# Kernel optimization log

Hardware: AMD Instinct MI355X
Metric: run time of the kernel (lower is better)

## Reference

```python
import jax, jax.numpy as jnp
import numpy as np

N_TYPES = 4
N_REL = 8
N_HEADS = 8
IN_DIM = 256
N_HID = 128
D_K = N_HID // N_HEADS
N_LAYERS = 2
N_NODES = 100000
N_EDGES = 400000


def setup_inputs() -> dict:
    key = jax.random.key(0)
    ks = jax.random.split(key, 24)
    s = 0.05
    inp = {
        'node_feature': jax.random.normal(ks[0], (N_NODES, IN_DIM), jnp.float32),
        'node_type': jax.random.randint(ks[1], (N_NODES,), 0, N_TYPES),
        'edge_index': jax.random.randint(ks[2], (2, N_EDGES), 0, N_NODES),
        'edge_type': jax.random.randint(ks[3], (N_EDGES,), 0, N_REL),
        # per-type input adapters
        'adapt_w': jax.random.normal(ks[4], (N_TYPES, IN_DIM, N_HID), jnp.float32) * s,
        'adapt_b': jnp.zeros((N_TYPES, N_HID), jnp.float32),
        # HGT conv params, stacked over layers
        'k_w': jax.random.normal(ks[5], (N_LAYERS, N_TYPES, N_HID, N_HID), jnp.float32) * s,
        'k_b': jnp.zeros((N_LAYERS, N_TYPES, N_HID), jnp.float32),
        'q_w': jax.random.normal(ks[6], (N_LAYERS, N_TYPES, N_HID, N_HID), jnp.float32) * s,
        'q_b': jnp.zeros((N_LAYERS, N_TYPES, N_HID), jnp.float32),
        'v_w': jax.random.normal(ks[7], (N_LAYERS, N_TYPES, N_HID, N_HID), jnp.float32) * s,
        'v_b': jnp.zeros((N_LAYERS, N_TYPES, N_HID), jnp.float32),
        'a_w': jax.random.normal(ks[8], (N_LAYERS, N_TYPES, N_HID, N_HID), jnp.float32) * s,
        'a_b': jnp.zeros((N_LAYERS, N_TYPES, N_HID), jnp.float32),
        'rel_pri': jnp.ones((N_LAYERS, N_REL, N_HEADS), jnp.float32),
        'rel_att': jnp.tile(jnp.eye(D_K, dtype=jnp.float32), (N_LAYERS, N_REL, N_HEADS, 1, 1))
                   + jax.random.normal(ks[9], (N_LAYERS, N_REL, N_HEADS, D_K, D_K), jnp.float32) * s,
        'rel_msg': jnp.tile(jnp.eye(D_K, dtype=jnp.float32), (N_LAYERS, N_REL, N_HEADS, 1, 1))
                   + jax.random.normal(ks[10], (N_LAYERS, N_REL, N_HEADS, D_K, D_K), jnp.float32) * s,
        'skip': jnp.ones((N_LAYERS, N_TYPES), jnp.float32),
    }
    return inp


def _per_type_linear(x, w, b, node_type, n_idx):
    # x: [N, din], w: [T, din, dout], b: [T, dout] -> gather row for each node's type
    h_all = jnp.einsum('ni,tio->tno', x, w) + b[:, None, :]  # [T, N, dout]
    return h_all[node_type, n_idx]  # [N, dout]


def _edge_softmax(score, tgt, n):
    # score: [E, H]; softmax over incoming edges of each target node
    m = jax.ops.segment_max(score, tgt, num_segments=n)  # [N, H]
    e = jnp.exp(score - m[tgt])
    z = jax.ops.segment_sum(e, tgt, num_segments=n)
    return e / (z[tgt] + 1e-9)


def _hgt_layer(x, node_type, src, tgt, edge_type,
               kw, kb, qw, qb, vw, vb, aw, ab, pri, att_m, msg_m, skip):
    n = x.shape[0]
    n_idx = jnp.arange(n)
    k = _per_type_linear(x, kw, kb, node_type, n_idx).reshape(n, N_HEADS, D_K)
    q = _per_type_linear(x, qw, qb, node_type, n_idx).reshape(n, N_HEADS, D_K)
    v = _per_type_linear(x, vw, vb, node_type, n_idx).reshape(n, N_HEADS, D_K)
    k_src, v_src, q_tgt = k[src], v[src], q[tgt]  # [E, H, dk]
    # per-relation attention/message transforms, accumulated over small fixed R
    k_rel = jnp.zeros_like(k_src)
    v_rel = jnp.zeros_like(v_src)
    for r in range(N_REL):
        msk = (edge_type == r)[:, None, None]
        k_rel = k_rel + jnp.einsum('ehd,hdf->ehf', jnp.where(msk, k_src, 0.0), att_m[r])
        v_rel = v_rel + jnp.einsum('ehd,hdf->ehf', jnp.where(msk, v_src, 0.0), msg_m[r])
    score = (q_tgt * k_rel).sum(-1) * pri[edge_type] * (1.0 / (D_K ** 0.5))  # [E, H]
    att = _edge_softmax(score, tgt, n)
    agg = jax.ops.segment_sum(att[..., None] * v_rel, tgt, num_segments=n)  # [N, H, dk]
    agg = agg.reshape(n, N_HID)
    trans = _per_type_linear(jax.nn.gelu(agg), aw, ab, node_type, n_idx)
    alpha = jax.nn.sigmoid(skip)[node_type][:, None]
    return trans * alpha + x * (1.0 - alpha)


def reference(node_feature, node_type, edge_index, edge_type,
              adapt_w, adapt_b, k_w, k_b, q_w, q_b, v_w, v_b,
              a_w, a_b, rel_pri, rel_att, rel_msg, skip):
    n = node_feature.shape[0]
    n_idx = jnp.arange(n)
    # per-node-type adapter + tanh (gather-linear-scatter, fully vectorized)
    h = jnp.tanh(_per_type_linear(node_feature, adapt_w, adapt_b, node_type, n_idx))
    src, tgt = edge_index[0], edge_index[1]
    for l in range(N_LAYERS):
        h = _hgt_layer(h, node_type, src, tgt, edge_type,
                       k_w[l], k_b[l], q_w[l], q_b[l], v_w[l], v_b[l],
                       a_w[l], a_b[l], rel_pri[l], rel_att[l], rel_msg[l], skip[l])
    return h
```

## Files before the change

### kernel.cpp

```cpp
#include <hip/hip_runtime.h>
#include <math.h>

constexpr int N_TYPES = 4;
constexpr int N_REL   = 8;
constexpr int N_HEADS = 8;
constexpr int IN_DIM  = 256;
constexpr int N_HID   = 128;
constexpr int D_K     = 16;
constexpr int N_LAYERS= 2;
constexpr int NN      = 100000;
constexpr int NE      = 400000;
constexpr int NBLK    = (NN + 255) / 256;

__device__ __forceinline__ float gelu_f(float x) {
    const float c = 0.7978845608028654f;
    float x3 = x * x * x;
    return 0.5f * x * (1.0f + tanhf(c * (x + 0.044715f * x3)));
}
__device__ __forceinline__ float sigmoid_f(float x) {
    return 1.0f / (1.0f + expf(-x));
}

__global__ __launch_bounds__(256) void count2_kernel(
    const int* __restrict__ ntype, const int* __restrict__ tgt,
    unsigned* ncnt, unsigned* tcnt)
{
    int i = blockIdx.x * 256 + threadIdx.x;
    int lane = threadIdx.x & 63;
    int t = (i < NN) ? ntype[i] : -1;
    #pragma unroll
    for (int tt = 0; tt < N_TYPES; tt++) {
        unsigned long long m = __ballot(t == tt);
        if (m != 0ull && lane == __ffsll((unsigned long long)m) - 1)
            atomicAdd(&ncnt[tt], (unsigned)__popcll(m));
    }
    if (i < NE) atomicAdd(&tcnt[tgt[i]], 1u);
}

__global__ void node_offsets_kernel(unsigned* c)
{
    unsigned a = 0;
    for (int t = 0; t < N_TYPES; t++) { c[8 + t] = a; c[4 + t] = a; a += c[t]; }
    c[8 + N_TYPES] = a;
}

__global__ __launch_bounds__(256) void scan1_kernel(
    const unsigned* __restrict__ cnt, unsigned* __restrict__ eoff,
    unsigned* __restrict__ bsum)
{
    __shared__ unsigned sh[256];
    int i = blockIdx.x * 256 + threadIdx.x;
    unsigned v = (i < NN) ? cnt[i] : 0u;
    sh[threadIdx.x] = v;
    __syncthreads();
    for (int off = 1; off < 256; off <<= 1) {
        unsigned add = (threadIdx.x >= off) ? sh[threadIdx.x - off] : 0u;
        __syncthreads();
        sh[threadIdx.x] += add;
        __syncthreads();
    }
    if (i < NN) eoff[i] = sh[threadIdx.x] - v;
    if (threadIdx.x == 255) bsum[blockIdx.x] = sh[255];
}

__global__ __launch_bounds__(512) void scan2_kernel(unsigned* __restrict__ bsum)
{
    __shared__ unsigned sh[512];
    int i = threadIdx.x;
    unsigned v = (i < NBLK) ? bsum[i] : 0u;
    sh[i] = v;
    __syncthreads();
    for (int off = 1; off < 512; off <<= 1) {
        unsigned add = (i >= off) ? sh[i - off] : 0u;
        __syncthreads();
        sh[i] += add;
        __syncthreads();
    }
    if (i < NBLK) bsum[i] = sh[i] - v;
}

__global__ __launch_bounds__(256) void scan3_kernel(
    unsigned* __restrict__ eoff, const unsigned* __restrict__ bsum,
    unsigned* __restrict__ ecur)
{
    int i = blockIdx.x * 256 + threadIdx.x;
    if (i < NN) {
        unsigned v = eoff[i] + bsum[blockIdx.x];
        eoff[i] = v;
        ecur[i] = v;
    }
    if (i == 0) eoff[NN] = (unsigned)NE;
}

__global__ __launch_bounds__(256) void scatter2_kernel(
    const int* __restrict__ ntype,
    const int* __restrict__ src, const int* __restrict__ tgt,
    const int* __restrict__ etype,
    unsigned* ncur, unsigned* ecur,
    int* __restrict__ nidx,
    int* __restrict__ er_t)
{
    int i = blockIdx.x * 256 + threadIdx.x;
    int lane = threadIdx.x & 63;
    int t = (i < NN) ? ntype[i] : -1;
    #pragma unroll
    for (int tt = 0; tt < N_TYPES; tt++) {
        unsigned long long m = __ballot(t == tt);
        if (m == 0ull) continue;
        int leader = __ffsll((unsigned long long)m) - 1;
        unsigned base = 0;
        if (lane == leader) base = atomicAdd(&ncur[tt], (unsigned)__popcll(m));
        base = __shfl(base, leader, 64);
        if (t == tt) {
            unsigned rank = (unsigned)__popcll(m & ((1ull << lane) - 1ull));
            nidx[base + rank] = i;
        }
    }
    if (i < NE) {
        int tg = tgt[i];
        unsigned p = atomicAdd(&ecur[tg], 1u);
        er_t[p] = (src[i] << 3) | etype[i];
    }
}

template<int DIN, int MIN, int MOUT>
__global__ __launch_bounds__(256) void ptl128_kernel(
    const float* __restrict__ x,
    const int* __restrict__ nidx,
    const unsigned* __restrict__ noff,
    const float* __restrict__ W,
    const float* __restrict__ Bb,
    const float* __restrict__ skipv,
    const float* __restrict__ hprev,
    float* __restrict__ out)
{
    constexpr int BK = 32;
    const int t = blockIdx.y;
    const unsigned s0 = noff[t], s1 = noff[t + 1];
    const unsigned base = s0 + blockIdx.x * 128u;
    if (base >= s1) return;
    const int nrows = (int)min(128u, s1 - base);

    __shared__ __align__(16) float xs[BK][128];
    __shared__ __align__(16) float wsl[BK][128];
    __shared__ int nid[128];

    const int tid = threadIdx.x;
    if (tid < 128) nid[tid] = nidx[base + (unsigned)min(tid, nrows - 1)];
    __syncthreads();

    const int tx = tid & 15;
    const int ty = tid >> 4;
    const int row = tid & 127, kg = tid >> 7;

    float acc[8][8];
    #pragma unroll
    for (int m = 0; m < 8; m++)
        #pragma unroll
        for (int j = 0; j < 8; j++) acc[m][j] = 0.0f;

    const float* Wt = W + (size_t)t * DIN * 128;

    for (int k0 = 0; k0 < DIN; k0 += BK) {
        {
            const float* xp = x + (size_t)nid[row] * DIN + k0 + kg * 16;
            float4 a0 = ((const float4*)xp)[0];
            float4 a1 = ((const float4*)xp)[1];
            float4 a2 = ((const float4*)xp)[2];
            float4 a3 = ((const float4*)xp)[3];
            float v[16] = {a0.x, a0.y, a0.z, a0.w, a1.x, a1.y, a1.z, a1.w,
                           a2.x, a2.y, a2.z, a2.w, a3.x, a3.y, a3.z, a3.w};
            #pragma unroll
            for (int i = 0; i < 16; i++) {
                float q = v[i];
                if (MIN == 1) q = gelu_f(q);
                xs[kg * 16 + i][row] = q;
            }
        }
        {
            const float* wp = Wt + (size_t)k0 * 128 + tid * 16;
            #pragma unroll
            for (int i = 0; i < 4; i++)
                *(float4*)&wsl[0][tid * 16 + 4 * i] = ((const float4*)wp)[i];
        }
        __syncthreads();
        #pragma unroll 8
        for (int kk = 0; kk < BK; kk++) {
            float4 xa = *(float4*)&xs[kk][ty * 8];
            float4 xb = *(float4*)&xs[kk][ty * 8 + 4];
            float4 wa = *(float4*)&wsl[kk][tx * 8];
            float4 wb = *(float4*)&wsl[kk][tx * 8 + 4];
            float xv[8] = {xa.x, xa.y, xa.z, xa.w, xb.x, xb.y, xb.z, xb.w};
            float wv[8] = {wa.x, wa.y, wa.z, wa.w, wb.x, wb.y, wb.z, wb.w};
            #pragma unroll
            for (int m = 0; m < 8; m++)
                #pragma unroll
                for (int j = 0; j < 8; j++)
                    acc[m][j] += xv[m] * wv[j];
        }
        __syncthreads();
    }

    float alpha = 0.0f;
    if (MOUT == 2) alpha = sigmoid_f(skipv[t]);
    float bb[8];
    #pragma unroll
    for (int j = 0; j < 8; j++) bb[j] = Bb[t * 128 + tx * 8 + j];

    #pragma unroll
    for (int m = 0; m < 8; m++) {
        int rr = ty * 8 + m;
        if (rr < nrows) {
            int n = nid[rr];
            float o[8];
            #pragma unroll
            for (int j = 0; j < 8; j++) o[j] = acc[m][j] + bb[j];
            if (MOUT == 0) {
                #pragma unroll
                for (int j = 0; j < 8; j++) o[j] = tanhf(o[j]);
            } else if (MOUT == 2) {
                const float* hp = hprev + (size_t)n * 128 + tx * 8;
                float4 h0 = *(const float4*)(hp);
                float4 h1 = *(const float4*)(hp + 4);
                float hv[8] = {h0.x, h0.y, h0.z, h0.w, h1.x, h1.y, h1.z, h1.w};
                #pragma unroll
                for (int j = 0; j < 8; j++)
                    o[j] = o[j] * alpha + hv[j] * (1.0f - alpha);
            }
            float* op = out + (size_t)n * 128 + tx * 8;
            *(float4*)(op)     = make_float4(o[0], o[1], o[2], o[3]);
            *(float4*)(op + 4) = make_float4(o[4], o[5], o[6], o[7]);
        }
    }
}

__global__ __launch_bounds__(256) void hgt_edge_fused(
    const int* __restrict__ er_t,
    const unsigned* __restrict__ eoff,
    const float* __restrict__ kbuf,
    const float* __restrict__ vbuf,
    const float* __restrict__ att,
    const float* __restrict__ msg,
    const float* __restrict__ pri,
    float* __restrict__ qagg)
{
    __shared__ float aq_lds[2][1024];
    __shared__ float pv_lds[2][1024];
    const int tid  = threadIdx.x;
    const int tsel = tid >> 7;
    const int li   = tid & 127;
    const int h    = li >> 4;
    const int j    = li & 15;
    const int l    = tid & 63;
    const int hb   = tid & 0x30;
    const int t    = blockIdx.x * 2 + tsel;
    if (t >= NN) return;

    const unsigned e0 = eoff[t];
    const unsigned e1 = eoff[t + 1];
    const int deg = (int)(e1 - e0);

    if (deg == 0) {
        qagg[(size_t)t * 128 + li] = 0.0f;
        return;
    }

    float* al = aq_lds[tsel];
    float* pl = pv_lds[tsel];

    #pragma unroll
    for (int r = 0; r < 8; r++) pl[r * 128 + li] = 0.0f;

    const float qo = qagg[(size_t)t * 128 + li];
    float qh[16];
    #pragma unroll
    for (int f = 0; f < 16; f++) qh[f] = __shfl(qo, hb + f, 64);

    int pkl = 0;
    if (l < 16 && e0 + (unsigned)l < e1) pkl = er_t[e0 + l];

    const int dc = min(deg, 16);
    unsigned mask = 0;
    for (int c = 0; c < dc; ++c) mask |= 1u << (__shfl(pkl, c, 64) & 7);
    for (unsigned e = e0 + 16; e < e1; ++e) mask |= 1u << (er_t[e] & 7);

    unsigned need = mask;
    while (need) {
        const int r = __ffs(need) - 1; need &= need - 1;
        const float* Ar = att + (((r * 8 + h) * 16 + j) * 16);
        float4 A0 = ((const float4*)Ar)[0];
        float4 A1 = ((const float4*)Ar)[1];
        float4 A2 = ((const float4*)Ar)[2];
        float4 A3 = ((const float4*)Ar)[3];
        float acc =
            A0.x*qh[0]  + A0.y*qh[1]  + A0.z*qh[2]  + A0.w*qh[3]  +
            A1.x*qh[4]  + A1.y*qh[5]  + A1.z*qh[6]  + A1.w*qh[7]  +
            A2.x*qh[8]  + A2.y*qh[9]  + A2.z*qh[10] + A2.w*qh[11] +
            A3.x*qh[12] + A3.y*qh[13] + A3.z*qh[14] + A3.w*qh[15];
        al[r * 128 + li] = acc * pri[r * 8 + h] * 0.25f;
    }

    float z = 0.0f;
    float* plp = pl + li;
    const float* alp = al + li;
    const float* kb = kbuf + li;
    const float* vb = vbuf + li;

    unsigned e = e0;
    for (; e + 4 <= e1; e += 4) {
        const int o = (int)(e - e0);
        int p0, p1, p2, p3;
        if (o + 3 < 16) {
            p0 = __shfl(pkl, o + 0, 64);
            p1 = __shfl(pkl, o + 1, 64);
            p2 = __shfl(pkl, o + 2, 64);
            p3 = __shfl(pkl, o + 3, 64);
        } else {
            p0 = er_t[e + 0]; p1 = er_t[e + 1];
            p2 = er_t[e + 2]; p3 = er_t[e + 3];
        }
        const int o0 = (p0 & ~7) << 4;
        const int o1 = (p1 & ~7) << 4;
        const int o2 = (p2 & ~7) << 4;
        const int o3 = (p3 & ~7) << 4;
        const float k0 = kb[o0]; const float v0 = vb[o0];
        const float k1 = kb[o1]; const float v1 = vb[o1];
        const float k2 = kb[o2]; const float v2 = vb[o2];
        const float k3 = kb[o3]; const float v3 = vb[o3];
        float s0 = k0 * alp[(p0 & 7) * 128];
        float s1 = k1 * alp[(p1 & 7) * 128];
        float s2 = k2 * alp[(p2 & 7) * 128];
        float s3 = k3 * alp[(p3 & 7) * 128];
        s0 += __shfl_xor(s0, 1); s1 += __shfl_xor(s1, 1);
        s2 += __shfl_xor(s2, 1); s3 += __shfl_xor(s3, 1);
        s0 += __shfl_xor(s0, 2); s1 += __shfl_xor(s1, 2);
        s2 += __shfl_xor(s2, 2); s3 += __shfl_xor(s3, 2);
        s0 += __shfl_xor(s0, 4); s1 += __shfl_xor(s1, 4);
        s2 += __shfl_xor(s2, 4); s3 += __shfl_xor(s3, 4);
        s0 += __shfl_xor(s0, 8); s1 += __shfl_xor(s1, 8);
        s2 += __shfl_xor(s2, 8); s3 += __shfl_xor(s3, 8);
        const float q0 = __expf(s0 - 8.0f);
        const float q1 = __expf(s1 - 8.0f);
        const float q2 = __expf(s2 - 8.0f);
        const float q3 = __expf(s3 - 8.0f);
        z += q0 + q1 + q2 + q3;
        plp[(p0 & 7) * 128] += q0 * v0;
        plp[(p1 & 7) * 128] += q1 * v1;
        plp[(p2 & 7) * 128] += q2 * v2;
        plp[(p3 & 7) * 128] += q3 * v3;
    }
    if (e + 2 <= e1) {
        const int o = (int)(e - e0);
        int p0, p1;
        if (o + 1 < 16) { p0 = __shfl(pkl, o, 64); p1 = __shfl(pkl, o + 1, 64); }
        else            { p0 = er_t[e]; p1 = er_t[e + 1]; }
        const int o0 = (p0 & ~7) << 4;
        const int o1 = (p1 & ~7) << 4;
        const float k0 = kb[o0]; const float v0 = vb[o0];
        const float k1 = kb[o1]; const float v1 = vb[o1];
        float s0 = k0 * alp[(p0 & 7) * 128];
        float s1 = k1 * alp[(p1 & 7) * 128];
        s0 += __shfl_xor(s0, 1); s1 += __shfl_xor(s1, 1);
        s0 += __shfl_xor(s0, 2); s1 += __shfl_xor(s1, 2);
        s0 += __shfl_xor(s0, 4); s1 += __shfl_xor(s1, 4);
        s0 += __shfl_xor(s0, 8); s1 += __shfl_xor(s1, 8);
        const float q0 = __expf(s0 - 8.0f);
        const float q1 = __expf(s1 - 8.0f);
        z += q0 + q1;
        plp[(p0 & 7) * 128] += q0 * v0;
        plp[(p1 & 7) * 128] += q1 * v1;
        e += 2;
    }
    if (e < e1) {
        const int o = (int)(e - e0);
        const int p0 = (o < 16) ? __shfl(pkl, o, 64) : er_t[e];
        const int o0 = (p0 & ~7) << 4;
        const float k0 = kb[o0]; const float v0 = vb[o0];
        float s0 = k0 * alp[(p0 & 7) * 128];
        s0 += __shfl_xor(s0, 1);
        s0 += __shfl_xor(s0, 2);
        s0 += __shfl_xor(s0, 4);
        s0 += __shfl_xor(s0, 8);
        const float q0 = __expf(s0 - 8.0f);
        z += q0;
        plp[(p0 & 7) * 128] += q0 * v0;
    }

    float acc = 0.0f;
    for (int r = 0; r < 8; r++) {
        if (!((mask >> r) & 1)) continue;
        const float* Mr = msg + ((r * 8 + h) * 256) + j;
        const float* sb = pl + r * 128 + h * 16;
        #pragma unroll
        for (int d = 0; d < 16; d++)
            acc += sb[d] * Mr[d * 16];
    }
    qagg[(size_t)t * 128 + li] = acc * __frcp_rn(z + 1e-9f);
}

extern "C" void kernel_launch(void* const* d_in, const int* in_sizes, int n_in,
                              void* d_out, int out_size, void* d_ws, size_t ws_size,
                              hipStream_t stream)
{
    const float* node_feature = (const float*)d_in[0];
    const int*   node_type    = (const int*)d_in[1];
    const int*   edge_index   = (const int*)d_in[2];
    const int*   edge_type    = (const int*)d_in[3];
    const float* adapt_w      = (const float*)d_in[4];
    const float* adapt_b      = (const float*)d_in[5];
    const float* k_w = (const float*)d_in[6];
    const float* k_b = (const float*)d_in[7];
    const float* q_w = (const float*)d_in[8];
    const float* q_b = (const float*)d_in[9];
    const float* v_w = (const float*)d_in[10];
    const float* v_b = (const float*)d_in[11];
    const float* a_w = (const float*)d_in[12];
    const float* a_b = (const float*)d_in[13];
    const float* rel_pri = (const float*)d_in[14];
    const float* rel_att = (const float*)d_in[15];
    const float* rel_msg = (const float*)d_in[16];
    const float* skip    = (const float*)d_in[17];

    const int* src = edge_index;
    const int* tgt = edge_index + NE;

    float* OUT = (float*)d_out;

    char* w = (char*)d_ws;
    auto alloc = [&](size_t bytes) -> void* {
        void* p = (void*)w;
        w += (bytes + 255) & ~(size_t)255;
        return p;
    };
    float*    B0    = (float*)alloc((size_t)NN * 128 * 4);
    float*    B1    = (float*)alloc((size_t)NN * 128 * 4);
    float*    B2    = (float*)alloc((size_t)NN * 128 * 4);
    int*      nidx  = (int*)alloc((size_t)NN * 4);
    int*      er_t  = (int*)alloc((size_t)NE * 4);
    unsigned* tcnt  = (unsigned*)alloc((size_t)NN * 4);
    unsigned* eoff  = (unsigned*)alloc((size_t)(NN + 1) * 4);
    unsigned* ecur  = (unsigned*)alloc((size_t)NN * 4);
    unsigned* bsum  = (unsigned*)alloc((size_t)NBLK * 4);
    unsigned* cnts  = (unsigned*)alloc(16 * 4);

    unsigned* ncnt = cnts;
    unsigned* ncur = cnts + 4;
    unsigned* noff = cnts + 8;

    hipMemsetAsync(cnts, 0, 16 * 4, stream);
    hipMemsetAsync(tcnt, 0, (size_t)NN * 4, stream);

    const int gblocks = (NE + 255) / 256;
    count2_kernel<<<gblocks, 256, 0, stream>>>(node_type, tgt, ncnt, tcnt);
    node_offsets_kernel<<<1, 1, 0, stream>>>(cnts);
    scan1_kernel<<<NBLK, 256, 0, stream>>>(tcnt, eoff, bsum);
    scan2_kernel<<<1, 512, 0, stream>>>(bsum);
    scan3_kernel<<<NBLK, 256, 0, stream>>>(eoff, bsum, ecur);
    scatter2_kernel<<<gblocks, 256, 0, stream>>>(node_type, src, tgt, edge_type,
                                                 ncur, ecur, nidx, er_t);

    dim3 pgrid((NN + 127) / 128, N_TYPES);
    ptl128_kernel<IN_DIM, 0, 0><<<pgrid, 256, 0, stream>>>(
        node_feature, nidx, noff, adapt_w, adapt_b, nullptr, nullptr, B0);

    const int fblocks = (NN + 1) / 2;

    for (int l = 0; l < N_LAYERS; l++) {
        float* hin  = l ? B1 : B0;
        float* kb_  = l ? B0 : B1;
        float* qb_  = B2;
        float* vb_  = OUT;
        float* hout = l ? OUT : B1;

        const float* kwl = k_w + (size_t)l * N_TYPES * 128 * 128;
        const float* kbl = k_b + (size_t)l * N_TYPES * 128;
        const float* qwl = q_w + (size_t)l * N_TYPES * 128 * 128;
        const float* qbl = q_b + (size_t)l * N_TYPES * 128;
        const float* vwl = v_w + (size_t)l * N_TYPES * 128 * 128;
        const float* vbl = v_b + (size_t)l * N_TYPES * 128;
        const float* awl = a_w + (size_t)l * N_TYPES * 128 * 128;
        const float* abl = a_b + (size_t)l * N_TYPES * 128;
        const float* pril = rel_pri + (size_t)l * N_REL * N_HEADS;
        const float* attl = rel_att + (size_t)l * N_REL * N_HEADS * D_K * D_K;
        const float* msgl = rel_msg + (size_t)l * N_REL * N_HEADS * D_K * D_K;
        const float* skipl = skip + (size_t)l * N_TYPES;

        ptl128_kernel<N_HID, 0, 1><<<pgrid, 256, 0, stream>>>(
            hin, nidx, noff, kwl, kbl, nullptr, nullptr, kb_);
        ptl128_kernel<N_HID, 0, 1><<<pgrid, 256, 0, stream>>>(
            hin, nidx, noff, qwl, qbl, nullptr, nullptr, qb_);
        ptl128_kernel<N_HID, 0, 1><<<pgrid, 256, 0, stream>>>(
            hin, nidx, noff, vwl, vbl, nullptr, nullptr, vb_);

        hgt_edge_fused<<<fblocks, 256, 0, stream>>>(
            er_t, eoff, kb_, vb_, attl, msgl, pril, qb_);

        ptl128_kernel<N_HID, 1, 2><<<pgrid, 256, 0, stream>>>(
            qb_, nidx, noff, awl, abl, skipl, hin, hout);
    }
}
```

Measured before the change: 1.205 ms.

## Run per-type 128-wide linears on bf16x3 MFMA with split hi/lo operands

Replaces the FP32 SIMT per-type linear kernels for K/Q/V and the output projection with an MFMA kernel. It keeps near-FP32 accuracy by splitting each operand into bf16 hi and lo parts and summing three products. Activations are converted (with GELU fused for the output projection) by a separate pass, and the weights are pre-transposed and split once per call. This targets the matrix-core throughput gap, at the cost of extra conversion passes and extra memory traffic for the split copies.

```diff
diff --git a/kernel.cpp b/kernel.cpp
--- a/kernel.cpp
+++ b/kernel.cpp
@@ -12,6 +12,9 @@
 constexpr int NE      = 400000;
 constexpr int NBLK    = (NN + 255) / 256;
 
+typedef __attribute__((ext_vector_type(8))) short bf16x8;
+typedef __attribute__((ext_vector_type(4))) float f32x4;
+
 __device__ __forceinline__ float gelu_f(float x) {
     const float c = 0.7978845608028654f;
     float x3 = x * x * x;
@@ -121,6 +124,54 @@
         unsigned p = atomicAdd(&ecur[tg], 1u);
         er_t[p] = (src[i] << 3) | etype[i];
     }
+}
+
+__device__ __forceinline__ void split_bf16(float q, ushort& hi, ushort& lo) {
+    unsigned u = __float_as_uint(q);
+    hi = (ushort)(u >> 16);
+    float hf = __uint_as_float(u & 0xFFFF0000u);
+    lo = (ushort)(__float_as_uint(q - hf) >> 16);
+}
+
+template<int GELU>
+__global__ __launch_bounds__(256) void cvt_x_kernel(
+    const float* __restrict__ x, ushort* __restrict__ xh,
+    ushort* __restrict__ xl, int total4)
+{
+    int gid = blockIdx.x * 256 + threadIdx.x;
+    if (gid >= total4) return;
+    float4 v = ((const float4*)x)[gid];
+    float a[4] = {v.x, v.y, v.z, v.w};
+    ushort h[4], lo[4];
+    #pragma unroll
+    for (int i = 0; i < 4; i++) {
+        float q = a[i];
+        if (GELU) q = gelu_f(q);
+        split_bf16(q, h[i], lo[i]);
+    }
+    uint2 hp, lp;
+    hp.x = (unsigned)h[0] | ((unsigned)h[1] << 16);
+    hp.y = (unsigned)h[2] | ((unsigned)h[3] << 16);
+    lp.x = (unsigned)lo[0] | ((unsigned)lo[1] << 16);
+    lp.y = (unsigned)lo[2] | ((unsigned)lo[3] << 16);
+    ((uint2*)xh)[gid] = hp;
+    ((uint2*)xl)[gid] = lp;
+}
+
+__global__ __launch_bounds__(256) void cvt_wT_kernel(
+    const float* __restrict__ W, ushort* __restrict__ whT,
+    ushort* __restrict__ wlT, int din)
+{
+    int gid = blockIdx.x * 256 + threadIdx.x;
+    int tot = 4 * din * 128;
+    if (gid >= tot) return;
+    int t = gid / (din * 128);
+    int rem = gid - t * din * 128;
+    int k = rem >> 7, n = rem & 127;
+    ushort hi, lo;
+    split_bf16(W[gid], hi, lo);
+    size_t o = ((size_t)t * 128 + n) * din + k;
+    whT[o] = hi; wlT[o] = lo;
 }
 
 template<int DIN, int MIN, int MOUT>
@@ -230,6 +281,111 @@
             float* op = out + (size_t)n * 128 + tx * 8;
             *(float4*)(op)     = make_float4(o[0], o[1], o[2], o[3]);
             *(float4*)(op + 4) = make_float4(o[4], o[5], o[6], o[7]);
+        }
+    }
+}
+
+template<int DIN, int MOUT>
+__global__ __launch_bounds__(256) void mfma_ptl_kernel(
+    const ushort* __restrict__ xh, const ushort* __restrict__ xl,
+    const int* __restrict__ nidx, const unsigned* __restrict__ noff,
+    const ushort* __restrict__ whT, const ushort* __restrict__ wlT,
+    const float* __restrict__ Bb,
+    const float* __restrict__ skipv, const float* __restrict__ hprev,
+    float* __restrict__ out)
+{
+    const int t = blockIdx.y;
+    const unsigned s0 = noff[t], s1 = noff[t + 1];
+    const unsigned base = s0 + blockIdx.x * 128u;
+    if (base >= s1) return;
+    const int nrows = (int)min(128u, s1 - base);
+
+    __shared__ __align__(16) ushort xsh[128][40];
+    __shared__ __align__(16) ushort xsl2[128][40];
+    __shared__ __align__(16) ushort wsh[128][40];
+    __shared__ __align__(16) ushort wsl2[128][40];
+    __shared__ int nid[128];
+
+    const int tid = threadIdx.x;
+    if (tid < 128) nid[tid] = nidx[base + (unsigned)min(tid, nrows - 1)];
+    __syncthreads();
+
+    const int lane = tid & 63;
+    const int wave = tid >> 6;
+    const int wr = wave >> 1, wc = wave & 1;
+    const int lm = lane & 15, lk = lane >> 4;
+
+    f32x4 acc[4][4];
+    #pragma unroll
+    for (int a = 0; a < 4; a++)
+        #pragma unroll
+        for (int b = 0; b < 4; b++)
+            acc[a][b] = (f32x4){0.0f, 0.0f, 0.0f, 0.0f};
+
+    const ushort* WhT = whT + (size_t)t * 128 * DIN;
+    const ushort* WlT = wlT + (size_t)t * 128 * DIN;
+
+    const int srow = tid & 127, shalf = tid >> 7;
+    const size_t xoff = (size_t)nid[srow] * DIN;
+
+    for (int k0 = 0; k0 < DIN; k0 += 32) {
+        {
+            const ushort* ph  = xh + xoff + k0 + shalf * 16;
+            const ushort* pl2 = xl + xoff + k0 + shalf * 16;
+            *(uint4*)&xsh[srow][shalf * 16]      = *(const uint4*)ph;
+            *(uint4*)&xsh[srow][shalf * 16 + 8]  = *(const uint4*)(ph + 8);
+            *(uint4*)&xsl2[srow][shalf * 16]     = *(const uint4*)pl2;
+            *(uint4*)&xsl2[srow][shalf * 16 + 8] = *(const uint4*)(pl2 + 8);
+            const ushort* qh = WhT + (size_t)srow * DIN + k0 + shalf * 16;
+            const ushort* ql = WlT + (size_t)srow * DIN + k0 + shalf * 16;
+            *(uint4*)&wsh[srow][shalf * 16]      = *(const uint4*)qh;
+            *(uint4*)&wsh[srow][shalf * 16 + 8]  = *(const uint4*)(qh + 8);
+            *(uint4*)&wsl2[srow][shalf * 16]     = *(const uint4*)ql;
+            *(uint4*)&wsl2[srow][shalf * 16 + 8] = *(const uint4*)(ql + 8);
+        }
+        __syncthreads();
+        bf16x8 ah[4], alo[4];
+        #pragma unroll
+        for (int fm = 0; fm < 4; fm++) {
+            int row = wr * 64 + fm * 16 + lm;
+            ah[fm]  = *(const bf16x8*)&xsh[row][lk * 8];
+            alo[fm] = *(const bf16x8*)&xsl2[row][lk * 8];
+        }
+        #pragma unroll
+        for (int fn = 0; fn < 4; fn++) {
+            int col = wc * 64 + fn * 16 + lm;
+            bf16x8 bh = *(const bf16x8*)&wsh[col][lk * 8];
+            bf16x8 bl = *(const bf16x8*)&wsl2[col][lk * 8];
+            #pragma unroll
+            for (int fm = 0; fm < 4; fm++) {
+                acc[fm][fn] = __builtin_amdgcn_mfma_f32_16x16x32_bf16(ah[fm],  bh, acc[fm][fn], 0, 0, 0);
+                acc[fm][fn] = __builtin_amdgcn_mfma_f32_16x16x32_bf16(ah[fm],  bl, acc[fm][fn], 0, 0, 0);
+                acc[fm][fn] = __builtin_amdgcn_mfma_f32_16x16x32_bf16(alo[fm], bh, acc[fm][fn], 0, 0, 0);
+            }
+        }
+        __syncthreads();
+    }
+
+    float alpha = 0.0f;
+    if (MOUT == 2) alpha = sigmoid_f(skipv[t]);
+    #pragma unroll
+    for (int fn = 0; fn < 4; fn++) {
+        const int dim = wc * 64 + fn * 16 + lm;
+        const float bias = Bb[t * 128 + dim];
+        #pragma unroll
+        for (int fm = 0; fm < 4; fm++) {
+            #pragma unroll
+            for (int i = 0; i < 4; i++) {
+                int rr = wr * 64 + fm * 16 + lk * 4 + i;
+                if (rr < nrows) {
+                    int n = nid[rr];
+                    float o = acc[fm][fn][i] + bias;
+                    if (MOUT == 0) o = tanhf(o);
+                    else if (MOUT == 2)
+                        o = o * alpha + hprev[(size_t)n * 128 + dim] * (1.0f - alpha);
+                    out[(size_t)n * 128 + dim] = o;
+                }
+            }
         }
     }
 }
@@ -435,6 +591,10 @@
     float*    B0    = (float*)alloc((size_t)NN * 128 * 4);
     float*    B1    = (float*)alloc((size_t)NN * 128 * 4);
     float*    B2    = (float*)alloc((size_t)NN * 128 * 4);
+    ushort*   XH    = (ushort*)alloc((size_t)NN * 128 * 2);
+    ushort*   XL    = (ushort*)alloc((size_t)NN * 128 * 2);
+    ushort*   WHT   = (ushort*)alloc((size_t)8 * 4 * 128 * 128 * 2);
+    ushort*   WLT   = (ushort*)alloc((size_t)8 * 4 * 128 * 128 * 2);
     int*      nidx  = (int*)alloc((size_t)NN * 4);
     int*      er_t  = (int*)alloc((size_t)NE * 4);
     unsigned* tcnt  = (unsigned*)alloc((size_t)NN * 4);
@@ -459,11 +619,25 @@
     scatter2_kernel<<<gblocks, 256, 0, stream>>>(node_type, src, tgt, edge_type,
                                                  ncur, ecur, nidx, er_t);
 
+    {
+        const int wtot = 4 * 128 * 128;
+        const int wblk = (wtot + 255) / 256;
+        const float* Ws[8] = {
+            k_w, q_w, v_w, a_w,
+            k_w + (size_t)wtot, q_w + (size_t)wtot,
+            v_w + (size_t)wtot, a_w + (size_t)wtot };
+        for (int m = 0; m < 8; m++)
+            cvt_wT_kernel<<<wblk, 256, 0, stream>>>(
+                Ws[m], WHT + (size_t)m * wtot, WLT + (size_t)m * wtot, 128);
+    }
+
     dim3 pgrid((NN + 127) / 128, N_TYPES);
     ptl128_kernel<IN_DIM, 0, 0><<<pgrid, 256, 0, stream>>>(
         node_feature, nidx, noff, adapt_w, adapt_b, nullptr, nullptr, B0);
 
     const int fblocks = (NN + 1) / 2;
+    const int cblocks = ((NN * 128 / 4) + 255) / 256;
+    const size_t wtot = (size_t)4 * 128 * 128;
 
     for (int l = 0; l < N_LAYERS; l++) {
         float* hin  = l ? B1 : B0;
@@ -472,30 +646,37 @@
         float* vb_  = OUT;
         float* hout = l ? OUT : B1;
 
-        const float* kwl = k_w + (size_t)l * N_TYPES * 128 * 128;
+        const ushort* khT = WHT + (size_t)(l * 4 + 0) * wtot;
+        const ushort* klT = WLT + (size_t)(l * 4 + 0) * wtot;
+        const ushort* qhT = WHT + (size_t)(l * 4 + 1) * wtot;
+        const ushort* qlT = WLT + (size_t)(l * 4 + 1) * wtot;
+        const ushort* vhT = WHT + (size_t)(l * 4 + 2) * wtot;
+        const ushort* vlT = WLT + (size_t)(l * 4 + 2) * wtot;
+        const ushort* ahT = WHT + (size_t)(l * 4 + 3) * wtot;
+        const ushort* alT = WLT + (size_t)(l * 4 + 3) * wtot;
+
         const float* kbl = k_b + (size_t)l * N_TYPES * 128;
-        const float* qwl = q_w + (size_t)l * N_TYPES * 128 * 128;
         const float* qbl = q_b + (size_t)l * N_TYPES * 128;
-        const float* vwl = v_w + (size_t)l * N_TYPES * 128 * 128;
         const float* vbl = v_b + (size_t)l * N_TYPES * 128;
-        const float* awl = a_w + (size_t)l * N_TYPES * 128 * 128;
         const float* abl = a_b + (size_t)l * N_TYPES * 128;
         const float* pril = rel_pri + (size_t)l * N_REL * N_HEADS;
         const float* attl = rel_att + (size_t)l * N_REL * N_HEADS * D_K * D_K;
         const float* msgl = rel_msg + (size_t)l * N_REL * N_HEADS * D_K * D_K;
         const float* skipl = skip + (size_t)l * N_TYPES;
 
-        ptl128_kernel<N_HID, 0, 1><<<pgrid, 256, 0, stream>>>(
-            hin, nidx, noff, kwl, kbl, nullptr, nullptr, kb_);
-        ptl128_kernel<N_HID, 0, 1><<<pgrid, 256, 0, stream>>>(
-            hin, nidx, noff, qwl, qbl, nullptr, nullptr, qb_);
-        ptl128_kernel<N_HID, 0, 1><<<pgrid, 256, 0, stream>>>(
-            hin, nidx, noff, vwl, vbl, nullptr, nullptr, vb_);
+        cvt_x_kernel<0><<<cblocks, 256, 0, stream>>>(hin, XH, XL, NN * 128 / 4);
+        mfma_ptl_kernel<128, 1><<<pgrid, 256, 0, stream>>>(
+            XH, XL, nidx, noff, khT, klT, kbl, nullptr, nullptr, kb_);
+        mfma_ptl_kernel<128, 1><<<pgrid, 256, 0, stream>>>(
+            XH, XL, nidx, noff, qhT, qlT, qbl, nullptr, nullptr, qb_);
+        mfma_ptl_kernel<128, 1><<<pgrid, 256, 0, stream>>>(
+            XH, XL, nidx, noff, vhT, vlT, vbl, nullptr, nullptr, vb_);
 
         hgt_edge_fused<<<fblocks, 256, 0, stream>>>(
             er_t, eoff, kb_, vb_, attl, msgl, pril, qb_);
 
-        ptl128_kernel<N_HID, 1, 2><<<pgrid, 256, 0, stream>>>(
-            qb_, nidx, noff, awl, abl, skipl, hin, hout);
-    }
-}
+        cvt_x_kernel<1><<<cblocks, 256, 0, stream>>>(qb_, XH, XL, NN * 128 / 4);
+        mfma_ptl_kernel<128, 2><<<pgrid, 256, 0, stream>>>(
+            XH, XL, nidx, noff, ahT, alT, abl, skipl, hin, hout);
+    }
+}
```

Result: slower. 1.256 ms (+4.3%).
